# Kernel tuning notes

Measured on AMD Instinct MI355X. Metric: run time of the kernel, lower is better.

Reference implementation:

```python
import jax, jax.numpy as jnp
import numpy as np

jax.config.update("jax_enable_x64", True)  # hash arithmetic needs int64 (mult*h ~ 1e10)

B, S, D, H = 8, 2048, 64, 8
NGRAMS = [2, 3, 4]
PRIMES = [100003, 100019, 100043]
VOCAB = 50257
TOTAL = len(NGRAMS) * H * D  # 1536


def setup_inputs() -> dict:
    key = jax.random.key(0)
    ks = jax.random.split(key, 16)
    # replicate MultiHeadHasher multipliers exactly (np.random.seed(42))
    np.random.seed(42)
    mults = [np.array([np.random.randint(2, p - 1) for _ in range(H)], dtype=np.int64)
             for p in PRIMES]
    inp = {}
    inp["token_ids"] = jax.random.randint(ks[0], (B, S), 0, VOCAB, dtype=jnp.int64)
    inp["hidden_states"] = jax.random.normal(ks[1], (B, S, D), dtype=jnp.float32)
    for i, (n, p) in enumerate(zip(NGRAMS, PRIMES)):
        # stacked per-head tables: [H, prime, D], init ~ N(0, 0.02^2) as in torch
        inp[f"table_n{n}"] = jax.random.normal(ks[2 + i], (H, p, D), dtype=jnp.float32) * 0.02
        inp[f"mult_n{n}"] = jnp.asarray(mults[i])
    # nn.Linear-style weights, stored as [in, out] so y = x @ W + b
    inp["Wq"] = jax.random.normal(ks[5], (D, D), dtype=jnp.float32) * (D ** -0.5)
    inp["bq"] = jnp.zeros((D,), dtype=jnp.float32)
    inp["Wk"] = jax.random.normal(ks[6], (TOTAL, D), dtype=jnp.float32) * (TOTAL ** -0.5)
    inp["bk"] = jnp.zeros((D,), dtype=jnp.float32)
    inp["Wv"] = jax.random.normal(ks[7], (TOTAL, D), dtype=jnp.float32) * (TOTAL ** -0.5)
    inp["bv"] = jnp.zeros((D,), dtype=jnp.float32)
    inp["Wo"] = jax.random.normal(ks[8], (D, D), dtype=jnp.float32) * (D ** -0.5)
    inp["bo"] = jnp.zeros((D,), dtype=jnp.float32)
    return inp


def _ngram_embed(tokens, mult, table, n, prime):
    """Rolling multiplicative hash of n-grams ending at each position, then gather.
    tokens: [B,S] int64; mult: [H] int64; table: [H,prime,D].
    Returns [B,S,H*D]; positions < n-1 are zeros (matches torch path).
    """
    Bb, Ss = tokens.shape
    pad = jnp.pad(tokens, ((0, 0), (n - 1, 0)))  # left-pad; masked out below
    h = jnp.zeros((Bb, 1, Ss), dtype=jnp.int64)
    for i in range(n):  # hash_val = (hash_val * mult + token) % prime
        t = pad[:, i:i + Ss]                       # token at pos p-(n-1-i)
        h = (h * mult[None, :, None] + t[:, None, :]) % prime  # [B,H,S]
    # per-head gather: table[h] -> [B,S,H,D]
    emb = jax.vmap(lambda tab, idx: tab[idx], in_axes=(0, 1), out_axes=2)(table, h)
    mask = (jnp.arange(Ss) >= n - 1).astype(emb.dtype)  # [S]
    emb = emb * mask[None, :, None, None]
    return emb.reshape(Bb, Ss, -1)  # n-major/head-minor matches torch concat order


def reference(token_ids, hidden_states,
              table_n2, mult_n2, table_n3, mult_n3, table_n4, mult_n4,
              Wq, bq, Wk, bk, Wv, bv, Wo, bo):
    mem = jnp.concatenate([
        _ngram_embed(token_ids, mult_n2, table_n2, 2, PRIMES[0]),
        _ngram_embed(token_ids, mult_n3, table_n3, 3, PRIMES[1]),
        _ngram_embed(token_ids, mult_n4, table_n4, 4, PRIMES[2]),
    ], axis=-1)  # [B,S,TOTAL]
    q = hidden_states @ Wq + bq          # [B,S,D]
    k = mem @ Wk + bk                    # [B,S,D]
    v = mem @ Wv + bv                    # [B,S,D]
    gate = jax.nn.sigmoid(jnp.sum(q * k, axis=-1, keepdims=True) / (D ** 0.5))
    out = (gate * v) @ Wo + bo           # gated + projected, [B,S,D]
    return (out, gate)
```

## Files before the change

### kernel.cpp

```cpp
#include <hip/hip_runtime.h>

#define SEQ  2048
#define NSEG 24

typedef __bf16 bf16x8 __attribute__((ext_vector_type(8)));
typedef float  f32x4  __attribute__((ext_vector_type(4)));
typedef unsigned short u16x4 __attribute__((ext_vector_type(4)));
typedef unsigned short ushort8 __attribute__((ext_vector_type(8)));
typedef unsigned long long u64;

#define WS_K 256
#define WS_V (256 + 196608)
#define WS_Q (256 + 393216)
#define WS_O (256 + 393216 + 8192)

__device__ __forceinline__ float4 ld4(const float* __restrict__ p) {
    return *reinterpret_cast<const float4*>(p);
}
__device__ __forceinline__ unsigned short f2bf(float f) {
    unsigned u = __float_as_uint(f);
    unsigned r = u + 0x7FFFu + ((u >> 16) & 1u);
    return (unsigned short)(r >> 16);
}

__global__ __launch_bounds__(256) void prep_ws(
    const float* __restrict__ Wk, const float* __restrict__ Wv,
    const float* __restrict__ Wq, const float* __restrict__ Wo,
    char* __restrict__ ws)
{
    const int tid = blockIdx.x * 256 + threadIdx.x;
    if (tid < 64) ((float*)ws)[tid] = 0.0f;
    const float* W; char* base; int it = tid;
    if      (it < 12288) { W = Wk; base = ws + WS_K; }
    else if (it < 24576) { W = Wv; base = ws + WS_V; it -= 12288; }
    else if (it < 25088) { W = Wq; base = ws + WS_Q; it -= 24576; }
    else if (it < 25600) { W = Wo; base = ws + WS_O; it -= 25088; }
    else return;
    const int lc = it & 15, lg = (it >> 4) & 3, nt = (it >> 6) & 3, sh = it >> 8;
    const int col = nt * 16 + lc;
    const int k0  = sh * 32 + lg * 8;
    ushort8 v;
#pragma unroll
    for (int j = 0; j < 8; ++j) v[j] = f2bf(W[(size_t)(k0 + j) * 64 + col]);
    *(ushort8*)(base + (size_t)it * 16) = v;
}

#define L_IDX  49152
#define LDS_BYTES 50688

__global__ __launch_bounds__(256, 3) void engram_main(
    const int*   __restrict__ tok,
    const float* __restrict__ hidden,
    const float* __restrict__ tab2, const int* __restrict__ mul2,
    const float* __restrict__ tab3, const int* __restrict__ mul3,
    const float* __restrict__ tab4, const int* __restrict__ mul4,
    const float* __restrict__ bq, const float* __restrict__ bk,
    const float* __restrict__ bv, const float* __restrict__ bo,
    const char*  __restrict__ ws,
    float* __restrict__ out, float* __restrict__ gate_out)
{
    __shared__ __align__(16) char L[LDS_BYTES];
    int*   idxL  = (int*)  (L + L_IDX);
    float* gatep = (float*)(L + L_IDX);
    float* gateL = (float*)(L + L_IDX + 256);
    char*  Lgv   = L;
    float* Lout  = (float*)(L + 4096);

    const int t     = threadIdx.x;
    const int pbase = blockIdx.x * 16;

    if (t < 128) {
        const int h = t >> 4, r = t & 15;
        const int pos = pbase + r;
        const int s   = pos & (SEQ - 1);
        const int b   = pos >> 11;
        const int* tr = tok + (size_t)b * SEQ;
        const u64 t3 = (u64)tr[s];
        const u64 t2 = (s >= 1) ? (u64)tr[s - 1] : 0ull;
        const u64 t1 = (s >= 2) ? (u64)tr[s - 2] : 0ull;
        const u64 t0 = (s >= 3) ? (u64)tr[s - 3] : 0ull;
        { u64 m = (u64)mul2[h];
          u64 hh = (t2 * m + t3) % 100003ull;
          idxL[h * 16 + r] = (s >= 1) ? (int)hh : -1; }
        { u64 m = (u64)mul3[h];
          u64 hh = (t1 * m + t2) % 100019ull;
          hh = (hh * m + t3) % 100019ull;
          idxL[(8 + h) * 16 + r] = (s >= 2) ? (int)hh : -1; }
        { u64 m = (u64)mul4[h];
          u64 hh = (t0 * m + t1) % 100043ull;
          hh = (hh * m + t2) % 100043ull;
          hh = (hh * m + t3) % 100043ull;
          idxL[(16 + h) * 16 + r] = (s >= 3) ? (int)hh : -1; }
    }
    __syncthreads();

    const int r     = t >> 4;
    const int c     = t & 15;
    const int fhalf = c >> 3, flg = (c >> 1) & 3, piece = c & 1;
    const int wb = fhalf * 1024 + flg * 256 + ((r ^ flg) << 4) + piece * 8;

    float4 R[NSEG];
#pragma unroll
    for (int s = 0; s < NSEG; ++s) {
        const int ix = idxL[s * 16 + r];
        const int ni = s >> 3, h = s & 7;
        const float* tabp; int prime;
        if (ni == 0)      { tabp = tab2; prime = 100003; }
        else if (ni == 1) { tabp = tab3; prime = 100019; }
        else              { tabp = tab4; prime = 100043; }
        float4 z; z.x = z.y = z.z = z.w = 0.0f;
        R[s] = (ix < 0) ? z : ld4(tabp + ((size_t)h * prime + ix) * 64 + c * 4);
    }
#pragma unroll
    for (int s = 0; s < NSEG; ++s) {
        u16x4 e;
        e[0] = f2bf(R[s].x); e[1] = f2bf(R[s].y);
        e[2] = f2bf(R[s].z); e[3] = f2bf(R[s].w);
        *(u16x4*)(L + s * 2048 + wb) = e;
    }
    __syncthreads();

    const int w   = t >> 6;
    const int lam = t & 63;
    const int lg  = lam >> 4, lc = lam & 15;
    const int fo  = lg * 256 + lc * 16;
    const int ra  = lg * 256 + (((lc ^ lg) & 15) << 4);

    const char* pK = ws + WS_K;
    const char* pV = ws + WS_V;
#define LOADB(s, k0_, k1_, v0_, v1_)                                     \
    { const char* bk_ = pK + (size_t)(s) * 8192 + w * 1024 + fo;         \
      const char* bv_ = pV + (size_t)(s) * 8192 + w * 1024 + fo;         \
      k0_ = *(const bf16x8*)(bk_);        k1_ = *(const bf16x8*)(bk_ + 4096); \
      v0_ = *(const bf16x8*)(bv_);        v1_ = *(const bf16x8*)(bv_ + 4096); }

    f32x4 kacc = {0.f,0.f,0.f,0.f}, vacc = {0.f,0.f,0.f,0.f};
    bf16x8 ck0, ck1, cv0, cv1, nk0, nk1, nv0, nv1;
    LOADB(0, ck0, ck1, cv0, cv1);
    LOADB(1, nk0, nk1, nv0, nv1);

    const float* hp = hidden + (size_t)(pbase + lc) * 64 + lg * 8;
    const float4 h0a = ld4(hp),      h0b = ld4(hp + 4);
    const float4 h1a = ld4(hp + 32), h1b = ld4(hp + 36);

#pragma unroll
    for (int s = 0; s < NSEG; ++s) {
        const bf16x8 a0 = *(const bf16x8*)(L + s * 2048 +        ra);
        const bf16x8 a1 = *(const bf16x8*)(L + s * 2048 + 1024 + ra);
        kacc = __builtin_amdgcn_mfma_f32_16x16x32_bf16(a0, ck0, kacc, 0, 0, 0);
        kacc = __builtin_amdgcn_mfma_f32_16x16x32_bf16(a1, ck1, kacc, 0, 0, 0);
        vacc = __builtin_amdgcn_mfma_f32_16x16x32_bf16(a0, cv0, vacc, 0, 0, 0);
        vacc = __builtin_amdgcn_mfma_f32_16x16x32_bf16(a1, cv1, vacc, 0, 0, 0);
        ck0 = nk0; ck1 = nk1; cv0 = nv0; cv1 = nv1;
        if (s + 2 < NSEG) LOADB(s + 2, nk0, nk1, nv0, nv1);
    }

    const int   cc  = w * 16 + lc;
    const float bkc = bk[cc], bvc = bv[cc], bqc = bq[cc], boc = bo[cc];
#pragma unroll
    for (int i = 0; i < 4; ++i) { kacc[i] += bkc; vacc[i] += bvc; }

    bf16x8 qa0, qa1;
    qa0[0]=(__bf16)h0a.x; qa0[1]=(__bf16)h0a.y; qa0[2]=(__bf16)h0a.z; qa0[3]=(__bf16)h0a.w;
    qa0[4]=(__bf16)h0b.x; qa0[5]=(__bf16)h0b.y; qa0[6]=(__bf16)h0b.z; qa0[7]=(__bf16)h0b.w;
    qa1[0]=(__bf16)h1a.x; qa1[1]=(__bf16)h1a.y; qa1[2]=(__bf16)h1a.z; qa1[3]=(__bf16)h1a.w;
    qa1[4]=(__bf16)h1b.x; qa1[5]=(__bf16)h1b.y; qa1[6]=(__bf16)h1b.z; qa1[7]=(__bf16)h1b.w;
    f32x4 qacc = {0.f,0.f,0.f,0.f};
    {
        const char* bq_ = ws + WS_Q + w * 1024 + fo;
        const bf16x8 qb0 = *(const bf16x8*)(bq_);
        const bf16x8 qb1 = *(const bf16x8*)(bq_ + 4096);
        qacc = __builtin_amdgcn_mfma_f32_16x16x32_bf16(qa0, qb0, qacc, 0, 0, 0);
        qacc = __builtin_amdgcn_mfma_f32_16x16x32_bf16(qa1, qb1, qacc, 0, 0, 0);
    }
    float gp4[4];
#pragma unroll
    for (int i = 0; i < 4; ++i) {
        float p = (qacc[i] + bqc) * kacc[i];
        p += __shfl_xor(p, 1, 64);
        p += __shfl_xor(p, 2, 64);
        p += __shfl_xor(p, 4, 64);
        p += __shfl_xor(p, 8, 64);
        gp4[i] = p;
    }
    if (lc == 0) {
#pragma unroll
        for (int i = 0; i < 4; ++i) gatep[w * 16 + lg * 4 + i] = gp4[i];
    }
    __syncthreads();

    if (t < 16) {
        const float s  = gatep[t] + gatep[16 + t] + gatep[32 + t] + gatep[48 + t];
        const float gt = 1.0f / (1.0f + expf(-s * 0.125f));
        gateL[t] = gt;
        gate_out[pbase + t] = gt;
    }
    __syncthreads();

#pragma unroll
    for (int i = 0; i < 4; ++i) {
        const int row = lg * 4 + i;
        const float gvv = gateL[row] * vacc[i];
        *(unsigned short*)(Lgv + row * 128 + ((w * 32 + lc * 2) ^ ((row & 7) << 4))) = f2bf(gvv);
    }
    __syncthreads();

    f32x4 oacc = {0.f,0.f,0.f,0.f};
    {
        const char* bo_ = ws + WS_O + w * 1024 + fo;
        const bf16x8 ob0 = *(const bf16x8*)(bo_);
        const bf16x8 ob1 = *(const bf16x8*)(bo_ + 4096);
        const bf16x8 ga0 = *(const bf16x8*)(Lgv + lc * 128 + ((lg * 16)      ^ ((lc & 7) << 4)));
        const bf16x8 ga1 = *(const bf16x8*)(Lgv + lc * 128 + ((64 + lg * 16) ^ ((lc & 7) << 4)));
        oacc = __builtin_amdgcn_mfma_f32_16x16x32_bf16(ga0, ob0, oacc, 0, 0, 0);
        oacc = __builtin_amdgcn_mfma_f32_16x16x32_bf16(ga1, ob1, oacc, 0, 0, 0);
    }
#pragma unroll
    for (int i = 0; i < 4; ++i)
        Lout[(lg * 4 + i) * 64 + cc] = oacc[i] + boc;
    __syncthreads();

    {
        const float4 o4 = *(const float4*)(Lout + r * 64 + c * 4);
        *reinterpret_cast<float4*>(out + (size_t)(pbase + r) * 64 + c * 4) = o4;
    }
}

extern "C" void kernel_launch(void* const* d_in, const int* in_sizes, int n_in,
                              void* d_out, int out_size, void* d_ws, size_t ws_size,
                              hipStream_t stream) {
    const int*   tok    = (const int*)  d_in[0];
    const float* hidden = (const float*)d_in[1];
    const float* tab2   = (const float*)d_in[2];
    const int*   mul2   = (const int*)  d_in[3];
    const float* tab3   = (const float*)d_in[4];
    const int*   mul3   = (const int*)  d_in[5];
    const float* tab4   = (const float*)d_in[6];
    const int*   mul4   = (const int*)  d_in[7];
    const float* Wq     = (const float*)d_in[8];
    const float* bq     = (const float*)d_in[9];
    const float* Wk     = (const float*)d_in[10];
    const float* bk     = (const float*)d_in[11];
    const float* Wv     = (const float*)d_in[12];
    const float* bv     = (const float*)d_in[13];
    const float* Wo     = (const float*)d_in[14];
    const float* bo     = (const float*)d_in[15];

    float* out      = (float*)d_out;
    float* gate_out = out + (size_t)16384 * 64;

    hipLaunchKernelGGL(prep_ws, dim3(100), dim3(256), 0, stream,
                       Wk, Wv, Wq, Wo, (char*)d_ws);
    hipLaunchKernelGGL(engram_main, dim3(16384 / 16), dim3(256), 0, stream,
                       tok, hidden, tab2, mul2, tab3, mul3, tab4, mul4,
                       bq, bk, bv, bo, (const char*)d_ws, out, gate_out);
}
```

Measured before the change: 40.35 us.

## Process two 16-row tiles per block with both gathers issued upfront

Each block now handles 32 positions as two 16-row tiles. It hashes indices for both tiles at once and issues the random table gathers for both tiles into two register arrays before any compute, so the second tile's gather latency overlaps the first tile's MFMA work. Grid size halves to 512 blocks and launch bounds drop from 3 to 2 blocks per CU to fit the doubled register footprint. The cost is fewer waves in flight and heavy register pressure from 48 float4 values held per thread.

```diff
diff --git a/kernel.cpp b/kernel.cpp
--- a/kernel.cpp
+++ b/kernel.cpp
@@ -46,9 +46,9 @@
 }
 
 #define L_IDX  49152
-#define LDS_BYTES 50688
-
-__global__ __launch_bounds__(256, 3) void engram_main(
+#define LDS_BYTES 52224
+
+__global__ __launch_bounds__(256, 2) void engram_main(
     const int*   __restrict__ tok,
     const float* __restrict__ hidden,
     const float* __restrict__ tab2, const int* __restrict__ mul2,
@@ -63,15 +63,14 @@
     int*   idxL  = (int*)  (L + L_IDX);
     float* gatep = (float*)(L + L_IDX);
     float* gateL = (float*)(L + L_IDX + 256);
-    char*  Lgv   = L;
-    float* Lout  = (float*)(L + 4096);
 
     const int t     = threadIdx.x;
-    const int pbase = blockIdx.x * 16;
-
-    if (t < 128) {
-        const int h = t >> 4, r = t & 15;
-        const int pos = pbase + r;
+    const int pbase = blockIdx.x * 32;
+
+    {
+        const int tile = t >> 7;
+        const int h = (t & 127) >> 4, r0 = t & 15;
+        const int pos = pbase + tile * 16 + r0;
         const int s   = pos & (SEQ - 1);
         const int b   = pos >> 11;
         const int* tr = tok + (size_t)b * SEQ;
@@ -79,18 +78,19 @@
         const u64 t2 = (s >= 1) ? (u64)tr[s - 1] : 0ull;
         const u64 t1 = (s >= 2) ? (u64)tr[s - 2] : 0ull;
         const u64 t0 = (s >= 3) ? (u64)tr[s - 3] : 0ull;
+        int* ix = idxL + tile * 384;
         { u64 m = (u64)mul2[h];
           u64 hh = (t2 * m + t3) % 100003ull;
-          idxL[h * 16 + r] = (s >= 1) ? (int)hh : -1; }
+          ix[h * 16 + r0] = (s >= 1) ? (int)hh : -1; }
         { u64 m = (u64)mul3[h];
           u64 hh = (t1 * m + t2) % 100019ull;
           hh = (hh * m + t3) % 100019ull;
-          idxL[(8 + h) * 16 + r] = (s >= 2) ? (int)hh : -1; }
+          ix[(8 + h) * 16 + r0] = (s >= 2) ? (int)hh : -1; }
         { u64 m = (u64)mul4[h];
           u64 hh = (t0 * m + t1) % 100043ull;
           hh = (hh * m + t2) % 100043ull;
           hh = (hh * m + t3) % 100043ull;
-          idxL[(16 + h) * 16 + r] = (s >= 3) ? (int)hh : -1; }
+          ix[(16 + h) * 16 + r0] = (s >= 3) ? (int)hh : -1; }
     }
     __syncthreads();
 
@@ -99,131 +99,148 @@
     const int fhalf = c >> 3, flg = (c >> 1) & 3, piece = c & 1;
     const int wb = fhalf * 1024 + flg * 256 + ((r ^ flg) << 4) + piece * 8;
 
-    float4 R[NSEG];
-#pragma unroll
-    for (int s = 0; s < NSEG; ++s) {
-        const int ix = idxL[s * 16 + r];
-        const int ni = s >> 3, h = s & 7;
-        const float* tabp; int prime;
-        if (ni == 0)      { tabp = tab2; prime = 100003; }
-        else if (ni == 1) { tabp = tab3; prime = 100019; }
-        else              { tabp = tab4; prime = 100043; }
-        float4 z; z.x = z.y = z.z = z.w = 0.0f;
-        R[s] = (ix < 0) ? z : ld4(tabp + ((size_t)h * prime + ix) * 64 + c * 4);
-    }
-#pragma unroll
-    for (int s = 0; s < NSEG; ++s) {
-        u16x4 e;
-        e[0] = f2bf(R[s].x); e[1] = f2bf(R[s].y);
-        e[2] = f2bf(R[s].z); e[3] = f2bf(R[s].w);
-        *(u16x4*)(L + s * 2048 + wb) = e;
-    }
-    __syncthreads();
+    float4 R1[NSEG], R2[NSEG];
+    auto gissue = [&](int tile, float4* R) {
+#pragma unroll
+        for (int s = 0; s < NSEG; ++s) {
+            const int ix = idxL[tile * 384 + s * 16 + r];
+            const int ni = s >> 3, h = s & 7;
+            const float* tabp; int prime;
+            if (ni == 0)      { tabp = tab2; prime = 100003; }
+            else if (ni == 1) { tabp = tab3; prime = 100019; }
+            else              { tabp = tab4; prime = 100043; }
+            float4 z; z.x = z.y = z.z = z.w = 0.0f;
+            R[s] = (ix < 0) ? z : ld4(tabp + ((size_t)h * prime + ix) * 64 + c * 4);
+        }
+    };
+    auto wbuf = [&](const float4* R) {
+#pragma unroll
+        for (int s = 0; s < NSEG; ++s) {
+            u16x4 e;
+            e[0] = f2bf(R[s].x); e[1] = f2bf(R[s].y);
+            e[2] = f2bf(R[s].z); e[3] = f2bf(R[s].w);
+            *(u16x4*)(L + s * 2048 + wb) = e;
+        }
+    };
+
+    gissue(0, R1);
+    gissue(1, R2);
 
     const int w   = t >> 6;
     const int lam = t & 63;
     const int lg  = lam >> 4, lc = lam & 15;
     const int fo  = lg * 256 + lc * 16;
     const int ra  = lg * 256 + (((lc ^ lg) & 15) << 4);
-
+    const int cc  = w * 16 + lc;
+    const float bkc = bk[cc], bvc = bv[cc], bqc = bq[cc], boc = bo[cc];
+
+    char*  Lgv  = L;
+    float* Lout = (float*)(L + 4096);
     const char* pK = ws + WS_K;
     const char* pV = ws + WS_V;
-#define LOADB(s, k0_, k1_, v0_, v1_)                                     \
-    { const char* bk_ = pK + (size_t)(s) * 8192 + w * 1024 + fo;         \
-      const char* bv_ = pV + (size_t)(s) * 8192 + w * 1024 + fo;         \
+#define LOADB(s, k0_, k1_, v0_, v1_)                                          \
+    { const char* bk_ = pK + (size_t)(s) * 8192 + w * 1024 + fo;              \
+      const char* bv_ = pV + (size_t)(s) * 8192 + w * 1024 + fo;              \
       k0_ = *(const bf16x8*)(bk_);        k1_ = *(const bf16x8*)(bk_ + 4096); \
       v0_ = *(const bf16x8*)(bv_);        v1_ = *(const bf16x8*)(bv_ + 4096); }
 
-    f32x4 kacc = {0.f,0.f,0.f,0.f}, vacc = {0.f,0.f,0.f,0.f};
-    bf16x8 ck0, ck1, cv0, cv1, nk0, nk1, nv0, nv1;
-    LOADB(0, ck0, ck1, cv0, cv1);
-    LOADB(1, nk0, nk1, nv0, nv1);
-
-    const float* hp = hidden + (size_t)(pbase + lc) * 64 + lg * 8;
-    const float4 h0a = ld4(hp),      h0b = ld4(hp + 4);
-    const float4 h1a = ld4(hp + 32), h1b = ld4(hp + 36);
-
-#pragma unroll
-    for (int s = 0; s < NSEG; ++s) {
-        const bf16x8 a0 = *(const bf16x8*)(L + s * 2048 +        ra);
-        const bf16x8 a1 = *(const bf16x8*)(L + s * 2048 + 1024 + ra);
-        kacc = __builtin_amdgcn_mfma_f32_16x16x32_bf16(a0, ck0, kacc, 0, 0, 0);
-        kacc = __builtin_amdgcn_mfma_f32_16x16x32_bf16(a1, ck1, kacc, 0, 0, 0);
-        vacc = __builtin_amdgcn_mfma_f32_16x16x32_bf16(a0, cv0, vacc, 0, 0, 0);
-        vacc = __builtin_amdgcn_mfma_f32_16x16x32_bf16(a1, cv1, vacc, 0, 0, 0);
-        ck0 = nk0; ck1 = nk1; cv0 = nv0; cv1 = nv1;
-        if (s + 2 < NSEG) LOADB(s + 2, nk0, nk1, nv0, nv1);
-    }
-
-    const int   cc  = w * 16 + lc;
-    const float bkc = bk[cc], bvc = bv[cc], bqc = bq[cc], boc = bo[cc];
-#pragma unroll
-    for (int i = 0; i < 4; ++i) { kacc[i] += bkc; vacc[i] += bvc; }
-
-    bf16x8 qa0, qa1;
-    qa0[0]=(__bf16)h0a.x; qa0[1]=(__bf16)h0a.y; qa0[2]=(__bf16)h0a.z; qa0[3]=(__bf16)h0a.w;
-    qa0[4]=(__bf16)h0b.x; qa0[5]=(__bf16)h0b.y; qa0[6]=(__bf16)h0b.z; qa0[7]=(__bf16)h0b.w;
-    qa1[0]=(__bf16)h1a.x; qa1[1]=(__bf16)h1a.y; qa1[2]=(__bf16)h1a.z; qa1[3]=(__bf16)h1a.w;
-    qa1[4]=(__bf16)h1b.x; qa1[5]=(__bf16)h1b.y; qa1[6]=(__bf16)h1b.z; qa1[7]=(__bf16)h1b.w;
-    f32x4 qacc = {0.f,0.f,0.f,0.f};
-    {
-        const char* bq_ = ws + WS_Q + w * 1024 + fo;
-        const bf16x8 qb0 = *(const bf16x8*)(bq_);
-        const bf16x8 qb1 = *(const bf16x8*)(bq_ + 4096);
-        qacc = __builtin_amdgcn_mfma_f32_16x16x32_bf16(qa0, qb0, qacc, 0, 0, 0);
-        qacc = __builtin_amdgcn_mfma_f32_16x16x32_bf16(qa1, qb1, qacc, 0, 0, 0);
-    }
-    float gp4[4];
-#pragma unroll
-    for (int i = 0; i < 4; ++i) {
-        float p = (qacc[i] + bqc) * kacc[i];
-        p += __shfl_xor(p, 1, 64);
-        p += __shfl_xor(p, 2, 64);
-        p += __shfl_xor(p, 4, 64);
-        p += __shfl_xor(p, 8, 64);
-        gp4[i] = p;
-    }
-    if (lc == 0) {
-#pragma unroll
-        for (int i = 0; i < 4; ++i) gatep[w * 16 + lg * 4 + i] = gp4[i];
-    }
-    __syncthreads();
-
-    if (t < 16) {
-        const float s  = gatep[t] + gatep[16 + t] + gatep[32 + t] + gatep[48 + t];
-        const float gt = 1.0f / (1.0f + expf(-s * 0.125f));
-        gateL[t] = gt;
-        gate_out[pbase + t] = gt;
-    }
-    __syncthreads();
-
-#pragma unroll
-    for (int i = 0; i < 4; ++i) {
-        const int row = lg * 4 + i;
-        const float gvv = gateL[row] * vacc[i];
-        *(unsigned short*)(Lgv + row * 128 + ((w * 32 + lc * 2) ^ ((row & 7) << 4))) = f2bf(gvv);
-    }
-    __syncthreads();
-
-    f32x4 oacc = {0.f,0.f,0.f,0.f};
-    {
-        const char* bo_ = ws + WS_O + w * 1024 + fo;
-        const bf16x8 ob0 = *(const bf16x8*)(bo_);
-        const bf16x8 ob1 = *(const bf16x8*)(bo_ + 4096);
-        const bf16x8 ga0 = *(const bf16x8*)(Lgv + lc * 128 + ((lg * 16)      ^ ((lc & 7) << 4)));
-        const bf16x8 ga1 = *(const bf16x8*)(Lgv + lc * 128 + ((64 + lg * 16) ^ ((lc & 7) << 4)));
-        oacc = __builtin_amdgcn_mfma_f32_16x16x32_bf16(ga0, ob0, oacc, 0, 0, 0);
-        oacc = __builtin_amdgcn_mfma_f32_16x16x32_bf16(ga1, ob1, oacc, 0, 0, 0);
-    }
-#pragma unroll
-    for (int i = 0; i < 4; ++i)
-        Lout[(lg * 4 + i) * 64 + cc] = oacc[i] + boc;
-    __syncthreads();
-
-    {
+    auto tileCompute = [&](int tile) {
+        f32x4 kacc = {0.f,0.f,0.f,0.f}, vacc = {0.f,0.f,0.f,0.f};
+        bf16x8 ck0, ck1, cv0, cv1, nk0, nk1, nv0, nv1;
+        LOADB(0, ck0, ck1, cv0, cv1);
+        LOADB(1, nk0, nk1, nv0, nv1);
+
+        const float* hp = hidden + (size_t)(pbase + tile * 16 + lc) * 64 + lg * 8;
+        const float4 h0a = ld4(hp),      h0b = ld4(hp + 4);
+        const float4 h1a = ld4(hp + 32), h1b = ld4(hp + 36);
+
+#pragma unroll
+        for (int s = 0; s < NSEG; ++s) {
+            const bf16x8 a0 = *(const bf16x8*)(L + s * 2048 +        ra);
+            const bf16x8 a1 = *(const bf16x8*)(L + s * 2048 + 1024 + ra);
+            kacc = __builtin_amdgcn_mfma_f32_16x16x32_bf16(a0, ck0, kacc, 0, 0, 0);
+            kacc = __builtin_amdgcn_mfma_f32_16x16x32_bf16(a1, ck1, kacc, 0, 0, 0);
+            vacc = __builtin_amdgcn_mfma_f32_16x16x32_bf16(a0, cv0, vacc, 0, 0, 0);
+            vacc = __builtin_amdgcn_mfma_f32_16x16x32_bf16(a1, cv1, vacc, 0, 0, 0);
+            ck0 = nk0; ck1 = nk1; cv0 = nv0; cv1 = nv1;
+            if (s + 2 < NSEG) LOADB(s + 2, nk0, nk1, nv0, nv1);
+        }
+
+#pragma unroll
+        for (int i = 0; i < 4; ++i) { kacc[i] += bkc; vacc[i] += bvc; }
+
+        bf16x8 qa0, qa1;
+        qa0[0]=(__bf16)h0a.x; qa0[1]=(__bf16)h0a.y; qa0[2]=(__bf16)h0a.z; qa0[3]=(__bf16)h0a.w;
+        qa0[4]=(__bf16)h0b.x; qa0[5]=(__bf16)h0b.y; qa0[6]=(__bf16)h0b.z; qa0[7]=(__bf16)h0b.w;
+        qa1[0]=(__bf16)h1a.x; qa1[1]=(__bf16)h1a.y; qa1[2]=(__bf16)h1a.z; qa1[3]=(__bf16)h1a.w;
+        qa1[4]=(__bf16)h1b.x; qa1[5]=(__bf16)h1b.y; qa1[6]=(__bf16)h1b.z; qa1[7]=(__bf16)h1b.w;
+        f32x4 qacc = {0.f,0.f,0.f,0.f};
+        {
+            const char* bq_ = ws + WS_Q + w * 1024 + fo;
+            const bf16x8 qb0 = *(const bf16x8*)(bq_);
+            const bf16x8 qb1 = *(const bf16x8*)(bq_ + 4096);
+            qacc = __builtin_amdgcn_mfma_f32_16x16x32_bf16(qa0, qb0, qacc, 0, 0, 0);
+            qacc = __builtin_amdgcn_mfma_f32_16x16x32_bf16(qa1, qb1, qacc, 0, 0, 0);
+        }
+        float gp4[4];
+#pragma unroll
+        for (int i = 0; i < 4; ++i) {
+            float p = (qacc[i] + bqc) * kacc[i];
+            p += __shfl_xor(p, 1, 64);
+            p += __shfl_xor(p, 2, 64);
+            p += __shfl_xor(p, 4, 64);
+            p += __shfl_xor(p, 8, 64);
+            gp4[i] = p;
+        }
+        if (lc == 0) {
+#pragma unroll
+            for (int i = 0; i < 4; ++i) gatep[w * 16 + lg * 4 + i] = gp4[i];
+        }
+        __syncthreads();
+
+        if (t < 16) {
+            const float s  = gatep[t] + gatep[16 + t] + gatep[32 + t] + gatep[48 + t];
+            const float gt = 1.0f / (1.0f + expf(-s * 0.125f));
+            gateL[t] = gt;
+            gate_out[pbase + tile * 16 + t] = gt;
+        }
+        __syncthreads();
+
+#pragma unroll
+        for (int i = 0; i < 4; ++i) {
+            const int row = lg * 4 + i;
+            const float gvv = gateL[row] * vacc[i];
+            *(unsigned short*)(Lgv + row * 128 + ((w * 32 + lc * 2) ^ ((row & 7) << 4))) = f2bf(gvv);
+        }
+        __syncthreads();
+
+        f32x4 oacc = {0.f,0.f,0.f,0.f};
+        {
+            const char* bo_ = ws + WS_O + w * 1024 + fo;
+            const bf16x8 ob0 = *(const bf16x8*)(bo_);
+            const bf16x8 ob1 = *(const bf16x8*)(bo_ + 4096);
+            const bf16x8 ga0 = *(const bf16x8*)(Lgv + lc * 128 + ((lg * 16)      ^ ((lc & 7) << 4)));
+            const bf16x8 ga1 = *(const bf16x8*)(Lgv + lc * 128 + ((64 + lg * 16) ^ ((lc & 7) << 4)));
+            oacc = __builtin_amdgcn_mfma_f32_16x16x32_bf16(ga0, ob0, oacc, 0, 0, 0);
+            oacc = __builtin_amdgcn_mfma_f32_16x16x32_bf16(ga1, ob1, oacc, 0, 0, 0);
+        }
+#pragma unroll
+        for (int i = 0; i < 4; ++i)
+            Lout[(lg * 4 + i) * 64 + cc] = oacc[i] + boc;
+        __syncthreads();
+
         const float4 o4 = *(const float4*)(Lout + r * 64 + c * 4);
-        *reinterpret_cast<float4*>(out + (size_t)(pbase + r) * 64 + c * 4) = o4;
-    }
+        *reinterpret_cast<float4*>(out + (size_t)(pbase + tile * 16 + r) * 64 + c * 4) = o4;
+    };
+
+    wbuf(R1);
+    __syncthreads();
+    tileCompute(0);
+    __syncthreads();
+
+    wbuf(R2);
+    __syncthreads();
+    tileCompute(1);
 }
 
 extern "C" void kernel_launch(void* const* d_in, const int* in_sizes, int n_in,
@@ -251,7 +268,7 @@
 
     hipLaunchKernelGGL(prep_ws, dim3(100), dim3(256), 0, stream,
                        Wk, Wv, Wq, Wo, (char*)d_ws);
-    hipLaunchKernelGGL(engram_main, dim3(16384 / 16), dim3(256), 0, stream,
+    hipLaunchKernelGGL(engram_main, dim3(512), dim3(256), 0, stream,
                        tok, hidden, tab2, mul2, tab3, mul3, tab4, mul4,
                        bq, bk, bv, bo, (const char*)d_ws, out, gate_out);
 }
```

After: 55.18 us. +36.8%, slower.

## Split gathered segment staging into two halves to halve LDS and raise occupancy

Applied to the files above, without the earlier changes.

The 24 gathered embedding segments are now staged through LDS in two halves of 12, reusing one 24KB buffer, with two extra barriers between them. Both halves' global gathers are issued up front, so the second half's loads overlap the first half's MFMA work. LDS use drops from about 50KB to about 26KB and launch bounds rise from 3 to 4 blocks per CU, aiming at higher occupancy. The costs are extra synchronisation and register pressure from holding 24 float4 gather results under a tighter register budget.

```diff
diff --git a/kernel.cpp b/kernel.cpp
--- a/kernel.cpp
+++ b/kernel.cpp
@@ -2,6 +2,7 @@
 
 #define SEQ  2048
 #define NSEG 24
+#define HSEG 12
 
 typedef __bf16 bf16x8 __attribute__((ext_vector_type(8)));
 typedef float  f32x4  __attribute__((ext_vector_type(4)));
@@ -45,10 +46,10 @@
     *(ushort8*)(base + (size_t)it * 16) = v;
 }
 
-#define L_IDX  49152
-#define LDS_BYTES 50688
-
-__global__ __launch_bounds__(256, 3) void engram_main(
+#define L_IDX  24576
+#define LDS_BYTES 26432
+
+__global__ __launch_bounds__(256, 4) void engram_main(
     const int*   __restrict__ tok,
     const float* __restrict__ hidden,
     const float* __restrict__ tab2, const int* __restrict__ mul2,
@@ -61,17 +62,15 @@
 {
     __shared__ __align__(16) char L[LDS_BYTES];
     int*   idxL  = (int*)  (L + L_IDX);
-    float* gatep = (float*)(L + L_IDX);
-    float* gateL = (float*)(L + L_IDX + 256);
-    char*  Lgv   = L;
-    float* Lout  = (float*)(L + 4096);
+    float* gatep = (float*)(L + L_IDX + 1536);
+    float* gateL = (float*)(L + L_IDX + 1792);
 
     const int t     = threadIdx.x;
     const int pbase = blockIdx.x * 16;
 
     if (t < 128) {
-        const int h = t >> 4, r = t & 15;
-        const int pos = pbase + r;
+        const int h = t >> 4, r0 = t & 15;
+        const int pos = pbase + r0;
         const int s   = pos & (SEQ - 1);
         const int b   = pos >> 11;
         const int* tr = tok + (size_t)b * SEQ;
@@ -81,16 +80,16 @@
         const u64 t0 = (s >= 3) ? (u64)tr[s - 3] : 0ull;
         { u64 m = (u64)mul2[h];
           u64 hh = (t2 * m + t3) % 100003ull;
-          idxL[h * 16 + r] = (s >= 1) ? (int)hh : -1; }
+          idxL[h * 16 + r0] = (s >= 1) ? (int)hh : -1; }
         { u64 m = (u64)mul3[h];
           u64 hh = (t1 * m + t2) % 100019ull;
           hh = (hh * m + t3) % 100019ull;
-          idxL[(8 + h) * 16 + r] = (s >= 2) ? (int)hh : -1; }
+          idxL[(8 + h) * 16 + r0] = (s >= 2) ? (int)hh : -1; }
         { u64 m = (u64)mul4[h];
           u64 hh = (t0 * m + t1) % 100043ull;
           hh = (hh * m + t2) % 100043ull;
           hh = (hh * m + t3) % 100043ull;
-          idxL[(16 + h) * 16 + r] = (s >= 3) ? (int)hh : -1; }
+          idxL[(16 + h) * 16 + r0] = (s >= 3) ? (int)hh : -1; }
     }
     __syncthreads();
 
@@ -99,64 +98,97 @@
     const int fhalf = c >> 3, flg = (c >> 1) & 3, piece = c & 1;
     const int wb = fhalf * 1024 + flg * 256 + ((r ^ flg) << 4) + piece * 8;
 
-    float4 R[NSEG];
-#pragma unroll
-    for (int s = 0; s < NSEG; ++s) {
-        const int ix = idxL[s * 16 + r];
-        const int ni = s >> 3, h = s & 7;
-        const float* tabp; int prime;
-        if (ni == 0)      { tabp = tab2; prime = 100003; }
-        else if (ni == 1) { tabp = tab3; prime = 100019; }
-        else              { tabp = tab4; prime = 100043; }
-        float4 z; z.x = z.y = z.z = z.w = 0.0f;
-        R[s] = (ix < 0) ? z : ld4(tabp + ((size_t)h * prime + ix) * 64 + c * 4);
-    }
-#pragma unroll
-    for (int s = 0; s < NSEG; ++s) {
-        u16x4 e;
-        e[0] = f2bf(R[s].x); e[1] = f2bf(R[s].y);
-        e[2] = f2bf(R[s].z); e[3] = f2bf(R[s].w);
-        *(u16x4*)(L + s * 2048 + wb) = e;
-    }
-    __syncthreads();
+    float4 R0[HSEG], R1[HSEG];
+    auto gissue = [&](int base, float4* R) {
+#pragma unroll
+        for (int sl = 0; sl < HSEG; ++sl) {
+            const int s  = base + sl;
+            const int ix = idxL[s * 16 + r];
+            const int ni = s >> 3, h = s & 7;
+            const float* tabp; int prime;
+            if (ni == 0)      { tabp = tab2; prime = 100003; }
+            else if (ni == 1) { tabp = tab3; prime = 100019; }
+            else              { tabp = tab4; prime = 100043; }
+            float4 z; z.x = z.y = z.z = z.w = 0.0f;
+            R[sl] = (ix < 0) ? z : ld4(tabp + ((size_t)h * prime + ix) * 64 + c * 4);
+        }
+    };
+    auto wbuf = [&](const float4* R) {
+#pragma unroll
+        for (int sl = 0; sl < HSEG; ++sl) {
+            u16x4 e;
+            e[0] = f2bf(R[sl].x); e[1] = f2bf(R[sl].y);
+            e[2] = f2bf(R[sl].z); e[3] = f2bf(R[sl].w);
+            *(u16x4*)(L + sl * 2048 + wb) = e;
+        }
+    };
+
+    gissue(0,    R0);
+    gissue(HSEG, R1);
 
     const int w   = t >> 6;
     const int lam = t & 63;
     const int lg  = lam >> 4, lc = lam & 15;
     const int fo  = lg * 256 + lc * 16;
     const int ra  = lg * 256 + (((lc ^ lg) & 15) << 4);
+    const int cc  = w * 16 + lc;
+    const float bkc = bk[cc], bvc = bv[cc], bqc = bq[cc], boc = bo[cc];
 
     const char* pK = ws + WS_K;
     const char* pV = ws + WS_V;
-#define LOADB(s, k0_, k1_, v0_, v1_)                                     \
-    { const char* bk_ = pK + (size_t)(s) * 8192 + w * 1024 + fo;         \
-      const char* bv_ = pV + (size_t)(s) * 8192 + w * 1024 + fo;         \
+#define LOADB(s, k0_, k1_, v0_, v1_)                                          \
+    { const char* bk_ = pK + (size_t)(s) * 8192 + w * 1024 + fo;              \
+      const char* bv_ = pV + (size_t)(s) * 8192 + w * 1024 + fo;              \
       k0_ = *(const bf16x8*)(bk_);        k1_ = *(const bf16x8*)(bk_ + 4096); \
       v0_ = *(const bf16x8*)(bv_);        v1_ = *(const bf16x8*)(bv_ + 4096); }
 
     f32x4 kacc = {0.f,0.f,0.f,0.f}, vacc = {0.f,0.f,0.f,0.f};
-    bf16x8 ck0, ck1, cv0, cv1, nk0, nk1, nv0, nv1;
-    LOADB(0, ck0, ck1, cv0, cv1);
-    LOADB(1, nk0, nk1, nv0, nv1);
-
-    const float* hp = hidden + (size_t)(pbase + lc) * 64 + lg * 8;
-    const float4 h0a = ld4(hp),      h0b = ld4(hp + 4);
-    const float4 h1a = ld4(hp + 32), h1b = ld4(hp + 36);
-
-#pragma unroll
-    for (int s = 0; s < NSEG; ++s) {
-        const bf16x8 a0 = *(const bf16x8*)(L + s * 2048 +        ra);
-        const bf16x8 a1 = *(const bf16x8*)(L + s * 2048 + 1024 + ra);
-        kacc = __builtin_amdgcn_mfma_f32_16x16x32_bf16(a0, ck0, kacc, 0, 0, 0);
-        kacc = __builtin_amdgcn_mfma_f32_16x16x32_bf16(a1, ck1, kacc, 0, 0, 0);
-        vacc = __builtin_amdgcn_mfma_f32_16x16x32_bf16(a0, cv0, vacc, 0, 0, 0);
-        vacc = __builtin_amdgcn_mfma_f32_16x16x32_bf16(a1, cv1, vacc, 0, 0, 0);
-        ck0 = nk0; ck1 = nk1; cv0 = nv0; cv1 = nv1;
-        if (s + 2 < NSEG) LOADB(s + 2, nk0, nk1, nv0, nv1);
-    }
-
-    const int   cc  = w * 16 + lc;
-    const float bkc = bk[cc], bvc = bv[cc], bqc = bq[cc], boc = bo[cc];
+    float4 h0a, h0b, h1a, h1b;
+
+    wbuf(R0);
+    __syncthreads();
+    {
+        bf16x8 ck0, ck1, cv0, cv1, nk0, nk1, nv0, nv1;
+        LOADB(0, ck0, ck1, cv0, cv1);
+        LOADB(1, nk0, nk1, nv0, nv1);
+
+        const float* hp = hidden + (size_t)(pbase + lc) * 64 + lg * 8;
+        h0a = ld4(hp);      h0b = ld4(hp + 4);
+        h1a = ld4(hp + 32); h1b = ld4(hp + 36);
+
+#pragma unroll
+        for (int sl = 0; sl < HSEG; ++sl) {
+            const bf16x8 a0 = *(const bf16x8*)(L + sl * 2048 +        ra);
+            const bf16x8 a1 = *(const bf16x8*)(L + sl * 2048 + 1024 + ra);
+            kacc = __builtin_amdgcn_mfma_f32_16x16x32_bf16(a0, ck0, kacc, 0, 0, 0);
+            kacc = __builtin_amdgcn_mfma_f32_16x16x32_bf16(a1, ck1, kacc, 0, 0, 0);
+            vacc = __builtin_amdgcn_mfma_f32_16x16x32_bf16(a0, cv0, vacc, 0, 0, 0);
+            vacc = __builtin_amdgcn_mfma_f32_16x16x32_bf16(a1, cv1, vacc, 0, 0, 0);
+            ck0 = nk0; ck1 = nk1; cv0 = nv0; cv1 = nv1;
+            if (sl + 2 < HSEG) LOADB(sl + 2, nk0, nk1, nv0, nv1);
+        }
+    }
+    __syncthreads();
+
+    wbuf(R1);
+    __syncthreads();
+    {
+        bf16x8 ck0, ck1, cv0, cv1, nk0, nk1, nv0, nv1;
+        LOADB(HSEG,     ck0, ck1, cv0, cv1);
+        LOADB(HSEG + 1, nk0, nk1, nv0, nv1);
+#pragma unroll
+        for (int sl = 0; sl < HSEG; ++sl) {
+            const bf16x8 a0 = *(const bf16x8*)(L + sl * 2048 +        ra);
+            const bf16x8 a1 = *(const bf16x8*)(L + sl * 2048 + 1024 + ra);
+            kacc = __builtin_amdgcn_mfma_f32_16x16x32_bf16(a0, ck0, kacc, 0, 0, 0);
+            kacc = __builtin_amdgcn_mfma_f32_16x16x32_bf16(a1, ck1, kacc, 0, 0, 0);
+            vacc = __builtin_amdgcn_mfma_f32_16x16x32_bf16(a0, cv0, vacc, 0, 0, 0);
+            vacc = __builtin_amdgcn_mfma_f32_16x16x32_bf16(a1, cv1, vacc, 0, 0, 0);
+            ck0 = nk0; ck1 = nk1; cv0 = nv0; cv1 = nv1;
+            if (sl + 2 < HSEG) LOADB(HSEG + sl + 2, nk0, nk1, nv0, nv1);
+        }
+    }
+
 #pragma unroll
     for (int i = 0; i < 4; ++i) { kacc[i] += bkc; vacc[i] += bvc; }
 
@@ -196,6 +228,9 @@
         gate_out[pbase + t] = gt;
     }
     __syncthreads();
+
+    char*  Lgv  = L;
+    float* Lout = (float*)(L + 4096);
 
 #pragma unroll
     for (int i = 0; i < 4; ++i) {
```

After: 41.26 us. 1.02x slower.
